# Kernel optimization log

Measured on AMD Instinct MI355X. Metric: run time of the kernel, lower is better.

Reference implementation:

```python
import jax, jax.numpy as jnp
import numpy as np

N = 8_000_000
THETA_W = 1.9  # physics-loss weight in forward()
EPS_DPDT = 1e-12
# Fixed config: bulk_modulus_model='tangent' (non-const), air_dissolution_model='on', air_fraction>0


def _drho_mix_dp(p, rho_L_atm, beta_L_atm, beta_gain, air_fraction, rho_g_atm,
                 polytropic_index, p_atm, p_crit, p_min):
    # mixture_density_derivative, vectorized over p (shape [N,1])
    p_used = jnp.maximum(p, p_min)
    L = p_crit - p_atm
    x = (p_used - p_atm) / L
    theta_mid = 1.0 - 3.0 * x**2 + 2.0 * x**3           # smoothstep between p_atm and p_crit
    theta = jnp.where(p_used <= p_atm, 1.0,
                      jnp.where(p_used >= p_crit, 0.0, theta_mid))
    dtheta_mid = 6.0 * (p_used - p_atm) * (p_used - p_crit) / L**3
    dtheta_dp = jnp.where((p_used <= p_atm) | (p_used >= p_crit), 0.0, dtheta_mid)

    afr = air_fraction / (1.0 - air_fraction)
    pr = (p_atm / p_used) ** (1.0 / polytropic_index)
    p_denom = afr * pr * theta
    p_ratio = afr * pr * (theta / (p_used * polytropic_index) - dtheta_dp)

    base = 1.0 + beta_gain * (p_used - p_atm) / beta_L_atm
    exp_term = base ** (-1.0 - 1.0 / beta_gain) / beta_L_atm

    rho_mix_init = rho_L_atm + rho_g_atm * afr
    denom = beta_L_atm * exp_term * base + p_denom
    return rho_mix_init * (exp_term + p_ratio) / denom**2


def setup_inputs() -> dict:
    key = jax.random.key(0)
    k1, k2, k3, k4 = jax.random.split(key, 4)
    outputs_P = jax.random.uniform(k1, (N, 1), dtype=jnp.float32) * 50.0  # p = 0.1*outputs_P in [0,5) MPa
    targets_P = outputs_P + 0.1 * jax.random.normal(k2, (N, 1), dtype=jnp.float32)
    dpdt = 0.5 * jax.random.normal(k3, (N, 1), dtype=jnp.float32)
    mdot_A = 0.01 * jax.random.normal(k4, (N, 1), dtype=jnp.float32)
    return {
        "targets_P": targets_P,
        "dpdt": dpdt,
        "mdot_A": mdot_A,
        "V": jnp.float32(1e-3),
        "outputs_P": outputs_P,
        "rho_L_atm": jnp.float32(850.0),
        "beta_L_atm": jnp.float32(1500.0),   # MPa
        "beta_gain": jnp.float32(10.0),
        "air_fraction": jnp.float32(0.005),
        "rho_g_atm": jnp.float32(1.2),
        "polytropic_index": jnp.float32(1.4),
        "p_atm": jnp.float32(0.101325),       # MPa
        "p_crit": jnp.float32(3.0),           # MPa
        "p_min": jnp.float32(0.01),           # MPa
    }


def reference(targets_P, dpdt, mdot_A, V, outputs_P, rho_L_atm, beta_L_atm,
              beta_gain, air_fraction, rho_g_atm, polytropic_index, p_atm,
              p_crit, p_min):
    drho = _drho_mix_dp(outputs_P * 0.1, rho_L_atm, beta_L_atm, beta_gain,
                        air_fraction, rho_g_atm, polytropic_index,
                        p_atm, p_crit, p_min)                      # [N,1]
    loss_physics = jnp.abs(V * drho * dpdt - mdot_A)                # [N,1]
    loss_M = jnp.abs(outputs_P - targets_P)                         # [N,1]
    per_sample = loss_M + THETA_W * loss_physics
    mask = jnp.abs(dpdt) >= EPS_DPDT                                # skip ~zero dpdt samples
    return jnp.sum(jnp.where(mask, per_sample, 0.0))
```

## Files before the change

kernel.cpp:

```cpp
#include <hip/hip_runtime.h>

#define THREADS 256

struct Consts {
    float p_min, p_atm, p_crit;
    float invL;
    float c_dth;
    float afr;
    float inv_n;
    float bg_over_bL;
    float inv_bL;
    float rho_mix_init;
    float V;
    float log2_patm;
    float pc1, pc2, pc3, pc4;
};

__device__ __forceinline__ float pow1p(float u, const Consts& c) {
    return fmaf(u, fmaf(u, fmaf(u, fmaf(u, c.pc4, c.pc3), c.pc2), c.pc1), 1.0f);
}

__device__ __forceinline__ float loss_elem(float oP, float tP, float dp, float md,
                                           const Consts& c) {
    float p  = 0.1f * oP;
    float pu = fmaxf(p, c.p_min);
    float dpa = pu - c.p_atm;
    float x = dpa * c.invL;
    float theta_mid = fmaf(x * x, fmaf(2.0f, x, -3.0f), 1.0f);
    bool lo = (pu <= c.p_atm);
    bool hi = (pu >= c.p_crit);
    float theta  = lo ? 1.0f : (hi ? 0.0f : theta_mid);
    float dtheta = (lo || hi) ? 0.0f : c.c_dth * dpa * (pu - c.p_crit);

    float inv_pu = __builtin_amdgcn_rcpf(pu);
    float lg_pu = __builtin_amdgcn_logf(pu);
    float pr = __builtin_amdgcn_exp2f(c.inv_n * (c.log2_patm - lg_pu));
    float apr = c.afr * pr;
    float p_denom = apr * theta;
    float p_ratio = apr * fmaf(theta * c.inv_n, inv_pu, -dtheta);

    float u  = dpa * c.bg_over_bL;
    float pb = pow1p(u, c);
    float exp_term = pb * c.inv_bL;
    float denom = fmaf(pb, u, pb) + p_denom;
    float inv_denom = __builtin_amdgcn_rcpf(denom);
    float drho = c.rho_mix_init * (exp_term + p_ratio) * inv_denom * inv_denom;

    float lp = fabsf(fmaf(c.V * dp, drho, -md));
    float lm = fabsf(oP - tP);
    float res = fmaf(1.9f, lp, lm);
    return (fabsf(dp) >= 1e-12f) ? res : 0.0f;
}

__global__ __launch_bounds__(THREADS) void loss_kernel(
    const float* __restrict__ targets_P,
    const float* __restrict__ dpdt,
    const float* __restrict__ mdot_A,
    const float* __restrict__ outputs_P,
    const float* __restrict__ sV,
    const float* __restrict__ s_rhoL,
    const float* __restrict__ s_betaL,
    const float* __restrict__ s_bgain,
    const float* __restrict__ s_airfr,
    const float* __restrict__ s_rhog,
    const float* __restrict__ s_poly,
    const float* __restrict__ s_patm,
    const float* __restrict__ s_pcrit,
    const float* __restrict__ s_pmin,
    float* __restrict__ partials,
    int n)
{
    const int n4  = n >> 2;
    const int idx = blockIdx.x * THREADS + threadIdx.x;
    const bool valid = idx < n4;
    const int s = valid ? idx : (n4 > 0 ? n4 - 1 : 0);

    const float4 o = ((const float4*)outputs_P)[s];
    const float4 t = ((const float4*)targets_P)[s];
    const float4 d = ((const float4*)dpdt)[s];
    const float4 m = ((const float4*)mdot_A)[s];

    Consts c;
    {
        float beta_L = *s_betaL;
        float bgain  = *s_bgain;
        float airfr  = *s_airfr;
        float poly   = *s_poly;
        float patm   = *s_patm;
        float pcrit  = *s_pcrit;
        float L = pcrit - patm;
        c.p_min = *s_pmin;
        c.p_atm = patm;
        c.p_crit = pcrit;
        c.invL = 1.0f / L;
        c.c_dth = 6.0f / (L * L * L);
        c.afr = airfr / (1.0f - airfr);
        c.inv_n = 1.0f / poly;
        c.bg_over_bL = bgain / beta_L;
        c.inv_bL = 1.0f / beta_L;
        c.rho_mix_init = fmaf(*s_rhog, c.afr, *s_rhoL);
        c.V = *sV;
        c.log2_patm = __builtin_amdgcn_logf(patm);
        float a = -1.0f - 1.0f / bgain;
        c.pc1 = a;
        c.pc2 = a * (a - 1.0f) * 0.5f;
        c.pc3 = c.pc2 * (a - 2.0f) * (1.0f / 3.0f);
        c.pc4 = c.pc3 * (a - 3.0f) * 0.25f;
    }

    float w = valid ? 1.0f : 0.0f;
    float sum = loss_elem(o.x, t.x, d.x, m.x, c)
              + loss_elem(o.y, t.y, d.y, m.y, c)
              + loss_elem(o.z, t.z, d.z, m.z, c)
              + loss_elem(o.w, t.w, d.w, m.w, c);
    float acc = w * sum;

    if (blockIdx.x == 0) {
        int j = (n4 << 2) + threadIdx.x;
        if (j < n)
            acc += loss_elem(outputs_P[j], targets_P[j], dpdt[j], mdot_A[j], c);
    }

    for (int off = 32; off > 0; off >>= 1)
        acc += __shfl_down(acc, off, 64);
    __shared__ float wsum[THREADS / 64];
    int lane = threadIdx.x & 63, wid = threadIdx.x >> 6;
    if (lane == 0) wsum[wid] = acc;
    __syncthreads();
    if (threadIdx.x == 0) {
        float bsum = 0.0f;
        #pragma unroll
        for (int v = 0; v < THREADS / 64; ++v) bsum += wsum[v];
        partials[blockIdx.x] = bsum;
    }
}

__global__ __launch_bounds__(256) void loss_final_kernel(
    const float* __restrict__ partials, float* __restrict__ out, int nparts)
{
    double acc = 0.0;
    for (int i = threadIdx.x; i < nparts; i += blockDim.x)
        acc += (double)partials[i];
    for (int off = 32; off > 0; off >>= 1)
        acc += __shfl_down(acc, off, 64);
    __shared__ double wsum[4];
    int lane = threadIdx.x & 63, wid = threadIdx.x >> 6;
    if (lane == 0) wsum[wid] = acc;
    __syncthreads();
    if (threadIdx.x == 0) {
        double s = 0.0;
        #pragma unroll
        for (int w = 0; w < 4; ++w) s += wsum[w];
        out[0] = (float)s;
    }
}

extern "C" void kernel_launch(void* const* d_in, const int* in_sizes, int n_in,
                              void* d_out, int out_size, void* d_ws, size_t ws_size,
                              hipStream_t stream) {
    const float* targets_P = (const float*)d_in[0];
    const float* dpdt      = (const float*)d_in[1];
    const float* mdot_A    = (const float*)d_in[2];
    const float* sV        = (const float*)d_in[3];
    const float* outputs_P = (const float*)d_in[4];
    const float* s_rhoL    = (const float*)d_in[5];
    const float* s_betaL   = (const float*)d_in[6];
    const float* s_bgain   = (const float*)d_in[7];
    const float* s_airfr   = (const float*)d_in[8];
    const float* s_rhog    = (const float*)d_in[9];
    const float* s_poly    = (const float*)d_in[10];
    const float* s_patm    = (const float*)d_in[11];
    const float* s_pcrit   = (const float*)d_in[12];
    const float* s_pmin    = (const float*)d_in[13];

    int n  = in_sizes[0];
    int n4 = n >> 2;
    int nblocks = (n4 + THREADS - 1) / THREADS;
    if (nblocks < 1) nblocks = 1;

    float* partials = (float*)d_ws;

    loss_kernel<<<nblocks, THREADS, 0, stream>>>(
        targets_P, dpdt, mdot_A, outputs_P,
        sV, s_rhoL, s_betaL, s_bgain, s_airfr, s_rhog, s_poly,
        s_patm, s_pcrit, s_pmin,
        partials, n);

    loss_final_kernel<<<1, 256, 0, stream>>>(partials, (float*)d_out, nblocks);
}
```

Before: 173.5 us.

## Process four float4 tiles per thread with double-buffered loads and sched barriers

Each thread now handles four float4 groups per array instead of one, and blocks drop to a quarter. Loads for the next group are issued before the current one is computed, and sched_barrier pins that order so memory latency overlaps with compute. Fewer blocks also shrinks the partials array and cuts the per-block constant setup and reduction overhead. A single tail block handles the leftover vectors and scalars serially, and the launch bound of 4 may limit register use.

```diff
diff --git a/kernel.cpp b/kernel.cpp
--- a/kernel.cpp
+++ b/kernel.cpp
@@ -1,6 +1,7 @@
 #include <hip/hip_runtime.h>
 
 #define THREADS 256
+#define ITER    4
 
 struct Consts {
     float p_min, p_atm, p_crit;
@@ -52,7 +53,51 @@
     return (fabsf(dp) >= 1e-12f) ? res : 0.0f;
 }
 
-__global__ __launch_bounds__(THREADS) void loss_kernel(
+__device__ __forceinline__ float quad(const float4& o, const float4& t,
+                                      const float4& d, const float4& m,
+                                      const Consts& c) {
+    return loss_elem(o.x, t.x, d.x, m.x, c)
+         + loss_elem(o.y, t.y, d.y, m.y, c)
+         + loss_elem(o.z, t.z, d.z, m.z, c)
+         + loss_elem(o.w, t.w, d.w, m.w, c);
+}
+
+__device__ __forceinline__ Consts make_consts(
+    const float* sV, const float* s_rhoL, const float* s_betaL,
+    const float* s_bgain, const float* s_airfr, const float* s_rhog,
+    const float* s_poly, const float* s_patm, const float* s_pcrit,
+    const float* s_pmin) {
+    Consts c;
+    float beta_L = *s_betaL;
+    float bgain  = *s_bgain;
+    float airfr  = *s_airfr;
+    float poly   = *s_poly;
+    float patm   = *s_patm;
+    float pcrit  = *s_pcrit;
+    float L = pcrit - patm;
+    c.p_min = *s_pmin;
+    c.p_atm = patm;
+    c.p_crit = pcrit;
+    c.invL = 1.0f / L;
+    c.c_dth = 6.0f / (L * L * L);
+    c.afr = airfr / (1.0f - airfr);
+    c.inv_n = 1.0f / poly;
+    c.bg_over_bL = bgain / beta_L;
+    c.inv_bL = 1.0f / beta_L;
+    c.rho_mix_init = fmaf(*s_rhog, c.afr, *s_rhoL);
+    c.V = *sV;
+    c.log2_patm = __builtin_amdgcn_logf(patm);
+    float a = -1.0f - 1.0f / bgain;
+    c.pc1 = a;
+    c.pc2 = a * (a - 1.0f) * 0.5f;
+    c.pc3 = c.pc2 * (a - 2.0f) * (1.0f / 3.0f);
+    c.pc4 = c.pc3 * (a - 3.0f) * 0.25f;
+    return c;
+}
+
+#define SB() __builtin_amdgcn_sched_barrier(0)
+
+__global__ __launch_bounds__(THREADS, 4) void loss_kernel(
     const float* __restrict__ targets_P,
     const float* __restrict__ dpdt,
     const float* __restrict__ mdot_A,
@@ -68,57 +113,51 @@
     const float* __restrict__ s_pcrit,
     const float* __restrict__ s_pmin,
     float* __restrict__ partials,
-    int n)
+    int n, int nfull)
 {
-    const int n4  = n >> 2;
-    const int idx = blockIdx.x * THREADS + threadIdx.x;
-    const bool valid = idx < n4;
-    const int s = valid ? idx : (n4 > 0 ? n4 - 1 : 0);
-
-    const float4 o = ((const float4*)outputs_P)[s];
-    const float4 t = ((const float4*)targets_P)[s];
-    const float4 d = ((const float4*)dpdt)[s];
-    const float4 m = ((const float4*)mdot_A)[s];
-
-    Consts c;
-    {
-        float beta_L = *s_betaL;
-        float bgain  = *s_bgain;
-        float airfr  = *s_airfr;
-        float poly   = *s_poly;
-        float patm   = *s_patm;
-        float pcrit  = *s_pcrit;
-        float L = pcrit - patm;
-        c.p_min = *s_pmin;
-        c.p_atm = patm;
-        c.p_crit = pcrit;
-        c.invL = 1.0f / L;
-        c.c_dth = 6.0f / (L * L * L);
-        c.afr = airfr / (1.0f - airfr);
-        c.inv_n = 1.0f / poly;
-        c.bg_over_bL = bgain / beta_L;
-        c.inv_bL = 1.0f / beta_L;
-        c.rho_mix_init = fmaf(*s_rhog, c.afr, *s_rhoL);
-        c.V = *sV;
-        c.log2_patm = __builtin_amdgcn_logf(patm);
-        float a = -1.0f - 1.0f / bgain;
-        c.pc1 = a;
-        c.pc2 = a * (a - 1.0f) * 0.5f;
-        c.pc3 = c.pc2 * (a - 2.0f) * (1.0f / 3.0f);
-        c.pc4 = c.pc3 * (a - 3.0f) * 0.25f;
-    }
-
-    float w = valid ? 1.0f : 0.0f;
-    float sum = loss_elem(o.x, t.x, d.x, m.x, c)
-              + loss_elem(o.y, t.y, d.y, m.y, c)
-              + loss_elem(o.z, t.z, d.z, m.z, c)
-              + loss_elem(o.w, t.w, d.w, m.w, c);
-    float acc = w * sum;
-
-    if (blockIdx.x == 0) {
-        int j = (n4 << 2) + threadIdx.x;
-        if (j < n)
+    const int n4 = n >> 2;
+    const float4* o4 = (const float4*)outputs_P;
+    const float4* t4 = (const float4*)targets_P;
+    const float4* d4 = (const float4*)dpdt;
+    const float4* m4 = (const float4*)mdot_A;
+
+    const Consts c = make_consts(sV, s_rhoL, s_betaL, s_bgain, s_airfr,
+                                 s_rhog, s_poly, s_patm, s_pcrit, s_pmin);
+
+    float acc = 0.0f;
+
+    if ((int)blockIdx.x < nfull) {
+        const int s0 = blockIdx.x * (THREADS * ITER) + threadIdx.x;
+        float4 oa, ta, da, ma, ob, tb, db, mb;
+
+        oa = o4[s0];              ta = t4[s0];
+        da = d4[s0];              ma = m4[s0];
+        SB();
+        ob = o4[s0 + THREADS];    tb = t4[s0 + THREADS];
+        db = d4[s0 + THREADS];    mb = m4[s0 + THREADS];
+        SB();
+        acc += quad(oa, ta, da, ma, c);
+        SB();
+        oa = o4[s0 + 2*THREADS];  ta = t4[s0 + 2*THREADS];
+        da = d4[s0 + 2*THREADS];  ma = m4[s0 + 2*THREADS];
+        SB();
+        acc += quad(ob, tb, db, mb, c);
+        SB();
+        ob = o4[s0 + 3*THREADS];  tb = t4[s0 + 3*THREADS];
+        db = d4[s0 + 3*THREADS];  mb = m4[s0 + 3*THREADS];
+        SB();
+        acc += quad(oa, ta, da, ma, c);
+        SB();
+        acc += quad(ob, tb, db, mb, c);
+    } else {
+        for (int idx = nfull * (THREADS * ITER) + threadIdx.x; idx < n4;
+             idx += THREADS) {
+            float4 oo = o4[idx], tt = t4[idx], dd = d4[idx], mm = m4[idx];
+            acc += quad(oo, tt, dd, mm, c);
+        }
+        for (int j = (n4 << 2) + threadIdx.x; j < n; j += THREADS) {
             acc += loss_elem(outputs_P[j], targets_P[j], dpdt[j], mdot_A[j], c);
+        }
     }
 
     for (int off = 32; off > 0; off >>= 1)
@@ -175,8 +214,8 @@
 
     int n  = in_sizes[0];
     int n4 = n >> 2;
-    int nblocks = (n4 + THREADS - 1) / THREADS;
-    if (nblocks < 1) nblocks = 1;
+    int nfull = n4 / (THREADS * ITER);
+    int nblocks = nfull + 1;
 
     float* partials = (float*)d_ws;
 
@@ -184,7 +223,7 @@
         targets_P, dpdt, mdot_A, outputs_P,
         sV, s_rhoL, s_betaL, s_bgain, s_airfr, s_rhog, s_poly,
         s_patm, s_pcrit, s_pmin,
-        partials, n);
+        partials, n, nfull);
 
     loss_final_kernel<<<1, 256, 0, stream>>>(partials, (float*)d_out, nblocks);
 }
```

Result: faster. 167.5 us (-3.5%).
